# Optimization experiments

Measured on AMD Instinct MI355X. Metric: run time of the kernel, lower is better.

## Reference

```python
import jax, jax.numpy as jnp
import numpy as np

DIM = 256
HEADS = 8
WS = 8      # window size
SS = 4      # shift size
EPS = 1e-5
HEAD_DIM = DIM // HEADS
SCALE = HEAD_DIM ** (-0.5)
N = WS * WS

# relative position index, replicating tf.meshgrid default 'xy' indexing
_ch = np.arange(WS)
_coords = np.stack(np.meshgrid(_ch, _ch, indexing='xy'))          # [2, WS, WS]
_flat = _coords.reshape(2, -1)                                     # [2, N]
_rel = _flat[:, :, None] - _flat[:, None, :]                       # [2, N, N]
_rel = _rel.transpose(1, 2, 0) + np.array([WS - 1, WS - 1])
_rel = _rel * np.array([2 * WS - 1, 1])
RPI = jnp.asarray(_rel.sum(-1).reshape(-1))                        # [N*N] int


def _calc_mask(H, W):
    # faithful to source: mask is -100 where window region ids are EQUAL, 0 otherwise
    img = np.zeros((H, W))
    slices = (slice(0, -WS), slice(-WS, -SS), slice(-SS, None))
    cnt = 0
    for hs in slices:
        for ws_ in slices:
            img[hs, ws_] = cnt
            cnt += 1
    mw = img.reshape(H // WS, WS, W // WS, WS).transpose(0, 2, 1, 3).reshape(-1, N)
    diff = mw[:, None, :] - mw[:, :, None]
    mask = np.where(diff == 0, -100.0, 0.0).astype(np.float32)     # [nW, N, N]
    return jnp.asarray(mask)


def _layernorm(x, g, b):
    m = jnp.mean(x, axis=-1, keepdims=True)
    v = jnp.mean(jnp.square(x - m), axis=-1, keepdims=True)
    return (x - m) * jax.lax.rsqrt(v + EPS) * g + b


def setup_inputs() -> dict:
    key = jax.random.key(0)
    ks = jax.random.split(key, 8)
    B, L, C = 16, 64 * 64, DIM
    s = 0.02
    return {
        'x': jax.random.normal(ks[0], (B, L, C), jnp.float32),
        'norm1_g': jnp.ones((C,), jnp.float32),
        'norm1_b': jnp.zeros((C,), jnp.float32),
        'qkv_w': jax.random.normal(ks[1], (C, 3 * C), jnp.float32) * s,
        'qkv_b': jnp.zeros((3 * C,), jnp.float32),
        'rpb_table': jax.random.normal(ks[2], ((2 * WS - 1) ** 2, HEADS), jnp.float32) * s,
        'proj_w': jax.random.normal(ks[3], (C, C), jnp.float32) * s,
        'proj_b': jnp.zeros((C,), jnp.float32),
        'norm2_g': jnp.ones((C,), jnp.float32),
        'norm2_b': jnp.zeros((C,), jnp.float32),
        'fc1_w': jax.random.normal(ks[4], (C, 4 * C), jnp.float32) * s,
        'fc1_b': jnp.zeros((4 * C,), jnp.float32),
        'fc2_w': jax.random.normal(ks[5], (4 * C, C), jnp.float32) * s,
        'fc2_b': jnp.zeros((C,), jnp.float32),
        'h': 64,
        'w': 64,
    }


def reference(x, norm1_g, norm1_b, qkv_w, qkv_b, rpb_table, proj_w, proj_b,
              norm2_g, norm2_b, fc1_w, fc1_b, fc2_w, fc2_b, h, w):
    B, L, C = x.shape
    nH, nW = h // WS, w // WS
    nWin = nH * nW
    shortcut = x

    xn = _layernorm(x, norm1_g, norm1_b).reshape(B, h, w, C)
    xn = jnp.roll(xn, shift=(-SS, -SS), axis=(1, 2))                 # cyclic shift
    # window partition -> [B*nWin, N, C]
    xw = xn.reshape(B, nH, WS, nW, WS, C).transpose(0, 1, 3, 2, 4, 5).reshape(B * nWin, N, C)

    qkv = (xw @ qkv_w + qkv_b).reshape(B * nWin, N, 3, HEADS, HEAD_DIM)
    qkv = qkv.transpose(2, 0, 3, 1, 4)                               # [3, B*nWin, H, N, d]
    q, k, v = qkv[0] * SCALE, qkv[1], qkv[2]

    attn = jnp.einsum('bhnd,bhmd->bhnm', q, k)                       # [B*nWin, H, N, N]
    bias = rpb_table[RPI].reshape(N, N, HEADS).transpose(2, 0, 1)    # [H, N, N]
    attn = attn + bias[None]

    mask = _calc_mask(h, w)                                          # [nWin, N, N]
    attn = attn.reshape(B, nWin, HEADS, N, N) + mask[None, :, None]
    attn = jax.nn.softmax(attn, axis=-1).reshape(B * nWin, HEADS, N, N)

    out = jnp.einsum('bhnm,bhmd->bhnd', attn, v)                     # [B*nWin, H, N, d]
    out = out.transpose(0, 2, 1, 3).reshape(B * nWin, N, C)
    out = out @ proj_w + proj_b

    # window reverse + reverse shift
    out = out.reshape(B, nH, nW, WS, WS, C).transpose(0, 1, 3, 2, 4, 5).reshape(B, h, w, C)
    out = jnp.roll(out, shift=(SS, SS), axis=(1, 2)).reshape(B, h * w, C)

    y = shortcut + out
    m = _layernorm(y, norm2_g, norm2_b)
    m = jax.nn.gelu(m @ fc1_w + fc1_b, approximate=False) @ fc2_w + fc2_b
    # faithful to source: final residual reuses the ORIGINAL shortcut, not y
    return shortcut + m
```

## Files before the change

kernel.cpp:

```cpp
#include <hip/hip_runtime.h>
#include <math.h>

typedef __bf16 bf16;
typedef __bf16 bf16x4 __attribute__((ext_vector_type(4)));
typedef __bf16 bf16x8 __attribute__((ext_vector_type(8)));
typedef float f32x4 __attribute__((ext_vector_type(4)));

#define AS1 __attribute__((address_space(1)))
#define AS3 __attribute__((address_space(3)))

__device__ __forceinline__ void gload_lds16(const bf16* g, bf16* l) {
    __builtin_amdgcn_global_load_lds((const AS1 void*)g, (AS3 void*)l, 16, 0, 0);
}
__device__ __forceinline__ void gload_lds16c(const char* g, char* l) {
    __builtin_amdgcn_global_load_lds((const AS1 void*)g, (AS3 void*)l, 16, 0, 0);
}

__device__ __forceinline__ float gelu_fast(float v) {
    const float u = 1.5957691216057308f * (v + 0.044715f * v * v * v);
    return v / (1.0f + __expf(-u));
}

__device__ __forceinline__ unsigned cvt_fp8x4(float a, float b, float c, float d) {
    int r = 0;
    r = __builtin_amdgcn_cvt_pk_fp8_f32(a, b, r, false);
    r = __builtin_amdgcn_cvt_pk_fp8_f32(c, d, r, true);
    return (unsigned)r;
}

__global__ __launch_bounds__(256)
void wprep_all(const float* __restrict__ qkv_w, const float* __restrict__ proj_w,
               const float* __restrict__ fc1_w, const float* __restrict__ fc2_w,
               bf16* __restrict__ qkv_wt, bf16* __restrict__ proj_wt,
               bf16* __restrict__ fc1_wt, char* __restrict__ fc2_wq)
{
    int idx = blockIdx.x * 256 + threadIdx.x;
    if (idx < 524288) {
        const float* src; bf16* dst; int K, N;
        if (idx < 196608)      { src = qkv_w;  dst = qkv_wt;  K = 256; N = 768; }
        else if (idx < 262144) { idx -= 196608; src = proj_w; dst = proj_wt; K = 256; N = 256; }
        else                   { idx -= 262144; src = fc1_w;  dst = fc1_wt;  K = 256; N = 1024; }
        const int k = idx / N, n = idx % N;
        dst[(long)n * K + k] = (bf16)src[idx];
    } else {
        idx -= 524288;
        const int k = idx >> 8, n = idx & 255;
        const int r = __builtin_amdgcn_cvt_pk_fp8_f32(fc2_w[idx] * 16.0f, 0.f, 0, false);
        fc2_wq[(long)n * 1024 + k] = (char)(r & 0xFF);
    }
}

__global__ __launch_bounds__(256)
void ln1_window(const float* __restrict__ x, const float* __restrict__ g,
                const float* __restrict__ be, bf16* __restrict__ xw)
{
    const int t = threadIdx.x;
    const int lane = t & 63;
    const int w = t >> 6;
    const long tok = (long)blockIdx.x * 4 + w;
    const float4 v = ((const float4*)(x + tok * 256))[lane];
    float sum = v.x + v.y + v.z + v.w;
    float sq  = v.x * v.x + v.y * v.y + v.z * v.z + v.w * v.w;
#pragma unroll
    for (int m = 32; m >= 1; m >>= 1) {
        sum += __shfl_xor(sum, m, 64);
        sq  += __shfl_xor(sq,  m, 64);
    }
    const float mean = sum * (1.0f / 256.0f);
    const float var  = sq * (1.0f / 256.0f) - mean * mean;
    const float rstd = rsqrtf(var + 1e-5f);
    const float4 gv = ((const float4*)g)[lane];
    const float4 bv = ((const float4*)be)[lane];
    bf16x4 ov;
    ov[0] = (bf16)((v.x - mean) * rstd * gv.x + bv.x);
    ov[1] = (bf16)((v.y - mean) * rstd * gv.y + bv.y);
    ov[2] = (bf16)((v.z - mean) * rstd * gv.z + bv.z);
    ov[3] = (bf16)((v.w - mean) * rstd * gv.w + bv.w);
    const int b = (int)(tok >> 12);
    const int l = (int)(tok & 4095);
    const int i = l >> 6, j = l & 63;
    const int ip = (i + 60) & 63, jp = (j + 60) & 63;
    const int winl = ((ip >> 3) << 3) + (jp >> 3);
    const int n = ((ip & 7) << 3) + (jp & 7);
    const long drow = ((long)b * 64 + winl) * 64 + n;
    *(bf16x4*)(xw + drow * 256 + lane * 4) = ov;
}

template<int EPI, int KT>
__global__ __launch_bounds__(512, 2)
void gemm_w(const bf16* __restrict__ A, const bf16* __restrict__ Bt,
            const float* __restrict__ bias, void* __restrict__ outp,
            int N, const float* __restrict__ xres, void* __restrict__ aux,
            int gx, int nb)
{
    constexpr int K = KT * 32;
    extern __shared__ bf16 lds[];
    bf16* sA = lds;
    bf16* sB = lds + 3 * 8192;
    const int t = threadIdx.x;
    const int l = t & 63;
    const int w = t >> 6;
    const int wr = w >> 1, wc = w & 1;
    const int q = nb >> 3;
    const int id = ((int)blockIdx.x & 7) * q + ((int)blockIdx.x >> 3);
    const long m0 = (long)(id / gx) * 256;
    const long n0 = (long)(id % gx) * 128;

    const bf16* asrcp[2]; bf16* adstp[2];
#pragma unroll
    for (int j = 0; j < 2; j++) {
        const int idx = j * 512 + t;
        const int p = idx >> 3, s = idx & 7;
        const int sl = s ^ (p & 7);
        const int row = 2 * p + (sl >> 2);
        const int ce = (sl & 3) * 8;
        asrcp[j] = A + (m0 + row) * (long)K + ce;
        adstp[j] = &sA[idx * 8];
    }
    const bf16* bsrcp; bf16* bdstp;
    {
        const int p = t >> 3, s = t & 7;
        const int sl = s ^ (p & 7);
        const int row = 2 * p + (sl >> 2);
        const int ce = (sl & 3) * 8;
        bsrcp = Bt + (n0 + row) * (long)K + ce;
        bdstp = &sB[t * 8];
    }

    const int c = l >> 4;
    int eA[4], eB[4];
#pragma unroll
    for (int i = 0; i < 4; i++) {
        const int rowA = wr * 64 + (l & 15) + i * 16;
        const int pa = rowA >> 1;
        eA[i] = (pa * 8 + ((((rowA & 1) << 2) + c) ^ (pa & 7))) * 8;
        const int rowB = wc * 64 + (l & 15) + i * 16;
        const int pb = rowB >> 1;
        eB[i] = (pb * 8 + ((((rowB & 1) << 2) + c) ^ (pb & 7))) * 8;
    }

    f32x4 acc[4][4];
#pragma unroll
    for (int i = 0; i < 4; i++)
#pragma unroll
        for (int j = 0; j < 4; j++) acc[i][j] = (f32x4){0.f, 0.f, 0.f, 0.f};

#define STAGE(bufi, ko)                                                        \
    do {                                                                       \
        gload_lds16(asrcp[0] + (ko), adstp[0] + (bufi) * 8192);                \
        gload_lds16(asrcp[1] + (ko), adstp[1] + (bufi) * 8192);                \
        gload_lds16(bsrcp + (ko), bdstp + (bufi) * 4096);                      \
    } while (0)

    STAGE(0, 0);
    STAGE(1, 32);

#pragma unroll
    for (int kt = 0; kt < KT; ++kt) {
        const int buf = kt % 3;
        if (kt < KT - 1)
            asm volatile("s_waitcnt vmcnt(3)" ::: "memory");
        else
            asm volatile("s_waitcnt vmcnt(0)" ::: "memory");
        __builtin_amdgcn_s_barrier();
        __builtin_amdgcn_sched_barrier(0);
        if (kt + 2 < KT)
            STAGE((kt + 2) % 3, (kt + 2) * 32);
        bf16x8 av[4], bv[4];
#pragma unroll
        for (int ni = 0; ni < 4; ni++)
            bv[ni] = *(const bf16x8*)&sB[buf * 4096 + eB[ni]];
#pragma unroll
        for (int mi = 0; mi < 4; mi++)
            av[mi] = *(const bf16x8*)&sA[buf * 8192 + eA[mi]];
#pragma unroll
        for (int mi = 0; mi < 4; mi++)
#pragma unroll
            for (int ni = 0; ni < 4; ni++)
                acc[mi][ni] = __builtin_amdgcn_mfma_f32_16x16x32_bf16(
                    bv[ni], av[mi], acc[mi][ni], 0, 0, 0);
    }
#undef STAGE

    if constexpr (EPI == 2) {
        __syncthreads();
        char* wlds = (char*)(lds) + w * 4608;
#pragma unroll
        for (int mi = 0; mi < 4; mi++)
#pragma unroll
            for (int ni = 0; ni < 4; ni++) {
                const int colb = ni * 16 + (l >> 4) * 4;
                const int rowl = mi * 16 + (l & 15);
                const float4 bz = *(const float4*)&bias[n0 + wc * 64 + colb];
                const unsigned pk = cvt_fp8x4(
                    gelu_fast(acc[mi][ni][0] + bz.x) * 16.0f,
                    gelu_fast(acc[mi][ni][1] + bz.y) * 16.0f,
                    gelu_fast(acc[mi][ni][2] + bz.z) * 16.0f,
                    gelu_fast(acc[mi][ni][3] + bz.w) * 16.0f);
                *(unsigned*)(wlds + rowl * 72 + colb) = pk;
            }
        char* outb = (char*)outp;
#pragma unroll
        for (int j = 0; j < 8; j++) {
            const int r = j * 8 + (l >> 3);
            const long vr = *(const long*)(wlds + r * 72 + (l & 7) * 8);
            const long row = m0 + wr * 64 + r;
            *(long*)&outb[row * (long)N + n0 + wc * 64 + (l & 7) * 8] = vr;
        }
    } else {
        const bool transpose_path = (n0 < 512);
        if (transpose_path) {
            __syncthreads();
            char* wlds = (char*)(lds) + w * 8704;
#pragma unroll
            for (int mi = 0; mi < 4; mi++)
#pragma unroll
                for (int ni = 0; ni < 4; ni++) {
                    const int colb = (ni * 16 + (l >> 4) * 4) * 2;
                    const int rowl = mi * 16 + (l & 15);
                    const float4 bz = *(const float4*)&bias[n0 + wc * 64 + ni * 16 + (l >> 4) * 4];
                    bf16x4 ov;
                    ov[0] = (bf16)(acc[mi][ni][0] + bz.x);
                    ov[1] = (bf16)(acc[mi][ni][1] + bz.y);
                    ov[2] = (bf16)(acc[mi][ni][2] + bz.z);
                    ov[3] = (bf16)(acc[mi][ni][3] + bz.w);
                    *(bf16x4*)(wlds + rowl * 136 + (colb ^ ((rowl & 7) << 4))) = ov;
                }
            bf16* outb = (bf16*)outp;
#pragma unroll
            for (int j = 0; j < 8; j++) {
                const int r = j * 8 + (l >> 3);
                const bf16x8 vr = *(const bf16x8*)(wlds + r * 136 + (((l & 7) * 16) ^ ((r & 7) << 4)));
                const long row = m0 + wr * 64 + r;
                const int col = (int)(n0 + wc * 64 + (l & 7) * 8);
                *(bf16x8*)&outb[row * N + col] = vr;
            }
        } else {
#pragma unroll
            for (int mi = 0; mi < 4; mi++)
#pragma unroll
                for (int ni = 0; ni < 4; ni++) {
                    const long row = m0 + wr * 64 + mi * 16 + (l & 15);
                    const int col = (int)(n0 + wc * 64 + ni * 16 + (l >> 4) * 4);
                    const float4 bz = *(const float4*)&bias[col];
                    bf16* vt = (bf16*)aux;
                    const int win = (int)(row >> 6);
                    const int n = (int)(row & 63);
#pragma unroll
                    for (int j = 0; j < 4; j++)
                        vt[(long)win * 16384 + (col - 512 + j) * 64 + n] =
                            (bf16)(acc[mi][ni][j] + ((const float*)&bz)[j]);
                }
        }
    }
    (void)xres; (void)aux;
}

__global__ __launch_bounds__(512, 2)
void gemm_fc2(const char* __restrict__ A, const char* __restrict__ Bq,
              const float* __restrict__ bias, float* __restrict__ out,
              const float* __restrict__ xres, int nb)
{
    constexpr int KT = 32;
    extern __shared__ char lds8[];
    char* sA8 = lds8;
    char* sB8 = lds8 + 3 * 8192;
    const int t = threadIdx.x;
    const int l = t & 63;
    const int w = t >> 6;
    const int wr = w >> 1, wc = w & 1;
    const int q = nb >> 3;
    const int id = ((int)blockIdx.x & 7) * q + ((int)blockIdx.x >> 3);
    const long m0 = (long)(id / 2) * 256;
    const long n0 = (long)(id % 2) * 128;

    const char* asrc; char* adst;
    {
        const int g = t >> 4, s = t & 15;
        const int r = s >> 1;
        const int h = (s & 1) ^ ((r >> 2) & 1);
        const int row = g * 8 + r;
        asrc = A + (m0 + row) * 1024 + h * 16;
        adst = sA8 + t * 16;
    }
    const char* bsrc = nullptr; char* bdst = nullptr;
    if (t < 256) {
        const int g = t >> 4, s = t & 15;
        const int r = s >> 1;
        const int h = (s & 1) ^ ((r >> 2) & 1);
        const int row = g * 8 + r;
        bsrc = Bq + (n0 + row) * 1024 + h * 16;
        bdst = sB8 + t * 16;
    }

    const int c = l >> 4;
    int eA[4], eB[4];
#pragma unroll
    for (int i = 0; i < 4; i++) {
        const int rowA = wr * 64 + (l & 15) + i * 16;
        const int rA = rowA & 7;
        eA[i] = (rowA >> 3) * 256 + (2 * rA + ((c >> 1) ^ ((rA >> 2) & 1))) * 16 + (c & 1) * 8;
        const int rowB = wc * 64 + (l & 15) + i * 16;
        const int rB = rowB & 7;
        eB[i] = (rowB >> 3) * 256 + (2 * rB + ((c >> 1) ^ ((rB >> 2) & 1))) * 16 + (c & 1) * 8;
    }

    f32x4 acc[4][4];
#pragma unroll
    for (int i = 0; i < 4; i++)
#pragma unroll
        for (int j = 0; j < 4; j++) acc[i][j] = (f32x4){0.f, 0.f, 0.f, 0.f};

#define STAGE2(bufi, ko)                                                       \
    do {                                                                       \
        gload_lds16c(asrc + (ko), adst + (bufi) * 8192);                       \
        if (t < 256) gload_lds16c(bsrc + (ko), bdst + (bufi) * 4096);          \
    } while (0)

    STAGE2(0, 0);
    STAGE2(1, 32);

#pragma unroll
    for (int kt = 0; kt < KT; ++kt) {
        const int buf = kt % 3;
        if (kt < KT - 1) {
            if (w < 4) asm volatile("s_waitcnt vmcnt(2)" ::: "memory");
            else       asm volatile("s_waitcnt vmcnt(1)" ::: "memory");
        } else {
            asm volatile("s_waitcnt vmcnt(0)" ::: "memory");
        }
        __builtin_amdgcn_s_barrier();
        __builtin_amdgcn_sched_barrier(0);
        if (kt + 2 < KT)
            STAGE2((kt + 2) % 3, (kt + 2) * 32);
        long av[4], bv[4];
#pragma unroll
        for (int ni = 0; ni < 4; ni++)
            bv[ni] = *(const long*)&sB8[buf * 4096 + eB[ni]];
#pragma unroll
        for (int mi = 0; mi < 4; mi++)
            av[mi] = *(const long*)&sA8[buf * 8192 + eA[mi]];
#pragma unroll
        for (int mi = 0; mi < 4; mi++)
#pragma unroll
            for (int ni = 0; ni < 4; ni++)
                acc[mi][ni] = __builtin_amdgcn_mfma_f32_16x16x32_fp8_fp8(
                    bv[ni], av[mi], acc[mi][ni], 0, 0, 0);
    }
#undef STAGE2

#pragma unroll
    for (int mi = 0; mi < 4; mi++)
#pragma unroll
        for (int ni = 0; ni < 4; ni++) {
            const long row = m0 + wr * 64 + mi * 16 + (l & 15);
            const int col = (int)(n0 + wc * 64 + ni * 16 + (l >> 4) * 4);
            const float4 bz = *(const float4*)&bias[col];
            const float4 xr = *(const float4*)&xres[row * 256 + col];
            float4 ov;
            ov.x = acc[mi][ni][0] * 0.00390625f + bz.x + xr.x;
            ov.y = acc[mi][ni][1] * 0.00390625f + bz.y + xr.y;
            ov.z = acc[mi][ni][2] * 0.00390625f + bz.z + xr.z;
            ov.w = acc[mi][ni][3] * 0.00390625f + bz.w + xr.w;
            *(float4*)&out[row * 256 + col] = ov;
        }
}

__global__ __launch_bounds__(512, 2)
void proj_ln2(const bf16* __restrict__ A, const bf16* __restrict__ Bt,
              const float* __restrict__ bias, const float* __restrict__ x,
              const float* __restrict__ g2, const float* __restrict__ b2,
              bf16* __restrict__ xn2, int nb)
{
    extern __shared__ bf16 lds[];
    bf16* sA = lds;
    bf16* sB = lds + 3 * 4096;
    float* sred = (float*)(lds + 3 * 4096 + 3 * 8192);
    const int t = threadIdx.x;
    const int l = t & 63;
    const int w = t >> 6;
    const int wr = w >> 2, wc = w & 3;
    const int q = nb >> 3;
    const int id = ((int)blockIdx.x & 7) * q + ((int)blockIdx.x >> 3);
    const long m0 = (long)id * 128;

    const bf16* asrcp; bf16* adstp;
    {
        const int p = t >> 3, s = t & 7;
        const int sl = s ^ (p & 7);
        const int row = 2 * p + (sl >> 2);
        const int ce = (sl & 3) * 8;
        asrcp = A + (m0 + row) * 256 + ce;
        adstp = &sA[t * 8];
    }
    const bf16* bsrcp[2]; bf16* bdstp[2];
#pragma unroll
    for (int j = 0; j < 2; j++) {
        const int idx = j * 512 + t;
        const int p = idx >> 3, s = idx & 7;
        const int sl = s ^ (p & 7);
        const int row = 2 * p + (sl >> 2);
        const int ce = (sl & 3) * 8;
        bsrcp[j] = Bt + (long)row * 256 + ce;
        bdstp[j] = &sB[idx * 8];
    }

    const int c = l >> 4;
    int eA[4], eB[4];
#pragma unroll
    for (int i = 0; i < 4; i++) {
        const int rowA = wr * 64 + (l & 15) + i * 16;
        const int pa = rowA >> 1;
        eA[i] = (pa * 8 + ((((rowA & 1) << 2) + c) ^ (pa & 7))) * 8;
        const int rowB = wc * 64 + (l & 15) + i * 16;
        const int pb = rowB >> 1;
        eB[i] = (pb * 8 + ((((rowB & 1) << 2) + c) ^ (pb & 7))) * 8;
    }

    f32x4 acc[4][4];
#pragma unroll
    for (int i = 0; i < 4; i++)
#pragma unroll
        for (int j = 0; j < 4; j++) acc[i][j] = (f32x4){0.f, 0.f, 0.f, 0.f};

#define STAGE(bufi, ko)                                                        \
    do {                                                                       \
        gload_lds16(asrcp + (ko), adstp + (bufi) * 4096);                      \
        gload_lds16(bsrcp[0] + (ko), bdstp[0] + (bufi) * 8192);                \
        gload_lds16(bsrcp[1] + (ko), bdstp[1] + (bufi) * 8192);                \
    } while (0)

    STAGE(0, 0);
    STAGE(1, 32);

#pragma unroll
    for (int kt = 0; kt < 8; ++kt) {
        const int buf = kt % 3;
        if (kt < 7)
            asm volatile("s_waitcnt vmcnt(3)" ::: "memory");
        else
            asm volatile("s_waitcnt vmcnt(0)" ::: "memory");
        __builtin_amdgcn_s_barrier();
        __builtin_amdgcn_sched_barrier(0);
        if (kt + 2 < 8)
            STAGE((kt + 2) % 3, (kt + 2) * 32);
        bf16x8 av[4], bv[4];
#pragma unroll
        for (int ni = 0; ni < 4; ni++)
            bv[ni] = *(const bf16x8*)&sB[buf * 8192 + eB[ni]];
#pragma unroll
        for (int mi = 0; mi < 4; mi++)
            av[mi] = *(const bf16x8*)&sA[buf * 4096 + eA[mi]];
#pragma unroll
        for (int mi = 0; mi < 4; mi++)
#pragma unroll
            for (int ni = 0; ni < 4; ni++)
                acc[mi][ni] = __builtin_amdgcn_mfma_f32_16x16x32_bf16(
                    bv[ni], av[mi], acc[mi][ni], 0, 0, 0);
    }
#undef STAGE

    float ts[4] = {0.f, 0.f, 0.f, 0.f}, tq[4] = {0.f, 0.f, 0.f, 0.f};
    long tok[4];
#pragma unroll
    for (int mi = 0; mi < 4; mi++) {
        const long row = m0 + wr * 64 + mi * 16 + (l & 15);
        const int gwin = (int)(row >> 6);
        const int n = (int)(row & 63);
        const int bb = gwin >> 6, wi = gwin & 63;
        const int ipp = ((wi >> 3) << 3) + (n >> 3);
        const int jpp = ((wi & 7) << 3) + (n & 7);
        const int ii = (ipp + 4) & 63, jj = (jpp + 4) & 63;
        tok[mi] = ((long)bb << 12) + (ii << 6) + jj;
#pragma unroll
        for (int ni = 0; ni < 4; ni++) {
            const int col = wc * 64 + ni * 16 + (l >> 4) * 4;
            const float4 bz = *(const float4*)&bias[col];
            const float4 xr = *(const float4*)&x[tok[mi] * 256 + col];
            acc[mi][ni][0] += bz.x + xr.x;
            acc[mi][ni][1] += bz.y + xr.y;
            acc[mi][ni][2] += bz.z + xr.z;
            acc[mi][ni][3] += bz.w + xr.w;
#pragma unroll
            for (int j = 0; j < 4; j++) {
                ts[mi] += acc[mi][ni][j];
                tq[mi] += acc[mi][ni][j] * acc[mi][ni][j];
            }
        }
    }
#pragma unroll
    for (int mi = 0; mi < 4; mi++) {
        ts[mi] += __shfl_xor(ts[mi], 16, 64);
        tq[mi] += __shfl_xor(tq[mi], 16, 64);
        ts[mi] += __shfl_xor(ts[mi], 32, 64);
        tq[mi] += __shfl_xor(tq[mi], 32, 64);
    }
    if (l < 16) {
#pragma unroll
        for (int mi = 0; mi < 4; mi++) {
            const int r = wr * 64 + mi * 16 + l;
            sred[r * 9 + wc * 2]     = ts[mi];
            sred[r * 9 + wc * 2 + 1] = tq[mi];
        }
    }
    __syncthreads();
#pragma unroll
    for (int mi = 0; mi < 4; mi++) {
        const int r = wr * 64 + mi * 16 + (l & 15);
        float S = 0.f, Q = 0.f;
#pragma unroll
        for (int k = 0; k < 4; k++) {
            S += sred[r * 9 + k * 2];
            Q += sred[r * 9 + k * 2 + 1];
        }
        const float mean = S * (1.0f / 256.0f);
        const float var  = Q * (1.0f / 256.0f) - mean * mean;
        const float rstd = rsqrtf(var + 1e-5f);
#pragma unroll
        for (int ni = 0; ni < 4; ni++) {
            const int col = wc * 64 + ni * 16 + (l >> 4) * 4;
            const float4 gg = *(const float4*)&g2[col];
            const float4 bb = *(const float4*)&b2[col];
            bf16x4 ov;
            ov[0] = (bf16)((acc[mi][ni][0] - mean) * rstd * gg.x + bb.x);
            ov[1] = (bf16)((acc[mi][ni][1] - mean) * rstd * gg.y + bb.y);
            ov[2] = (bf16)((acc[mi][ni][2] - mean) * rstd * gg.z + bb.z);
            ov[3] = (bf16)((acc[mi][ni][3] - mean) * rstd * gg.w + bb.w);
            *(bf16x4*)&xn2[tok[mi] * 256 + col] = ov;
        }
    }
}

__global__ __launch_bounds__(256, 4)
void attn_kernel(const bf16* __restrict__ qkv, const bf16* __restrict__ vT,
                 const float* __restrict__ rpb, bf16* __restrict__ out)
{
    __shared__ bf16 P_lds[4][64 * 64];
    const int t = threadIdx.x;
    const int lane = t & 63;
    const int w = t >> 6;
    const int win = blockIdx.x >> 1;
    const int head = (blockIdx.x & 1) * 4 + w;
    const int wi = win & 63;
    const int lr = lane & 15;
    const int lg = lane >> 4;
    const int lk = lg * 8;
    const long base = (long)win * 64 * 768;
    const float scale = 0.17677669529663687f;
    const int whb = (wi >> 3) << 3;
    const int wwb = (wi & 7) << 3;
    const f32x4 z4 = {0.f, 0.f, 0.f, 0.f};

    const bf16* qp  = qkv + base + head * 32;
    const bf16* kp  = qkv + base + 256 + head * 32;
    const bf16* vtp = vT + (long)win * 16384 + head * 32 * 64;

    int idm[4];
#pragma unroll
    for (int ni = 0; ni < 4; ni++) {
        const int m = ni * 16 + lr;
        const int gi2 = whb + (m >> 3), gj2 = wwb + (m & 7);
        idm[ni] = (gi2 < 56 ? 0 : (gi2 < 60 ? 1 : 2)) * 3 + (gj2 < 56 ? 0 : (gj2 < 60 ? 1 : 2));
    }

    bf16x8 aq[4], bk[4];
#pragma unroll
    for (int mi = 0; mi < 4; mi++)
        aq[mi] = *(const bf16x8*)(qp + (mi * 16 + lr) * 768 + lk);
#pragma unroll
    for (int ni = 0; ni < 4; ni++)
        bk[ni] = *(const bf16x8*)(kp + (ni * 16 + lr) * 768 + lk);

    f32x4 s[4][4];
#pragma unroll
    for (int i = 0; i < 4; i++)
#pragma unroll
        for (int j = 0; j < 4; j++) s[i][j] = z4;
#pragma unroll
    for (int mi = 0; mi < 4; mi++)
#pragma unroll
        for (int ni = 0; ni < 4; ni++)
            s[mi][ni] = __builtin_amdgcn_mfma_f32_16x16x32_bf16(aq[mi], bk[ni], s[mi][ni], 0, 0, 0);

#pragma unroll
    for (int mi = 0; mi < 4; mi++)
#pragma unroll
        for (int r = 0; r < 4; r++) {
            const int n = mi * 16 + lg * 4 + r;
            const int gi = whb + (n >> 3);
            const int gj = wwb + (n & 7);
            const int idn = (gi < 56 ? 0 : (gi < 60 ? 1 : 2)) * 3 + (gj < 56 ? 0 : (gj < 60 ? 1 : 2));
            float vals[4];
            float rowmax = -3.0e38f;
#pragma unroll
            for (int ni = 0; ni < 4; ni++) {
                const int m = ni * 16 + lr;
                const int dj = (n & 7) - (m & 7);
                const int di = (n >> 3) - (m >> 3);
                float sv = s[mi][ni][r] * scale + rpb[((dj + 7) * 15 + (di + 7)) * 8 + head];
                if (idn == idm[ni]) sv -= 100.0f;
                vals[ni] = sv;
                rowmax = fmaxf(rowmax, sv);
            }
#pragma unroll
            for (int msk = 8; msk >= 1; msk >>= 1)
                rowmax = fmaxf(rowmax, __shfl_xor(rowmax, msk, 64));
            float rsum = 0.f;
#pragma unroll
            for (int ni = 0; ni < 4; ni++) {
                const float p = __expf(vals[ni] - rowmax);
                vals[ni] = p;
                rsum += p;
            }
#pragma unroll
            for (int msk = 8; msk >= 1; msk >>= 1)
                rsum += __shfl_xor(rsum, msk, 64);
            const float inv = 1.0f / rsum;
            const int swz = (n & 7) << 3;
#pragma unroll
            for (int ni = 0; ni < 4; ni++)
                P_lds[w][n * 64 + ((ni * 16 + lr) ^ swz)] = (bf16)(vals[ni] * inv);
        }

    f32x4 o[4][2];
#pragma unroll
    for (int i = 0; i < 4; i++)
#pragma unroll
        for (int j = 0; j < 2; j++) o[i][j] = z4;
#pragma unroll
    for (int kk = 0; kk < 2; kk++) {
        bf16x8 bv[2];
#pragma unroll
        for (int ni = 0; ni < 2; ni++)
            bv[ni] = *(const bf16x8*)&vtp[(ni * 16 + lr) * 64 + kk * 32 + lk];
#pragma unroll
        for (int mi = 0; mi < 4; mi++) {
            const int row = mi * 16 + lr;
            const bf16x8 ap = *(const bf16x8*)&P_lds[w][row * 64 + ((kk * 32 + lk) ^ ((row & 7) << 3))];
#pragma unroll
            for (int ni = 0; ni < 2; ni++)
                o[mi][ni] = __builtin_amdgcn_mfma_f32_16x16x32_bf16(bv[ni], ap, o[mi][ni], 0, 0, 0);
        }
    }
#pragma unroll
    for (int mi = 0; mi < 4; mi++)
#pragma unroll
        for (int ni = 0; ni < 2; ni++) {
            const int n = mi * 16 + lr;
            const int d = ni * 16 + lg * 4;
            bf16x4 ov;
            ov[0] = (bf16)o[mi][ni][0]; ov[1] = (bf16)o[mi][ni][1];
            ov[2] = (bf16)o[mi][ni][2]; ov[3] = (bf16)o[mi][ni][3];
            *(bf16x4*)(out + ((long)(win * 64 + n)) * 256 + head * 32 + d) = ov;
        }
}

extern "C" void kernel_launch(void* const* d_in, const int* in_sizes, int n_in,
                              void* d_out, int out_size, void* d_ws, size_t ws_size,
                              hipStream_t stream)
{
    (void)in_sizes; (void)n_in; (void)out_size;
    const float* x      = (const float*)d_in[0];
    const float* n1g    = (const float*)d_in[1];
    const float* n1b    = (const float*)d_in[2];
    const float* qkv_w  = (const float*)d_in[3];
    const float* qkv_b  = (const float*)d_in[4];
    const float* rpb    = (const float*)d_in[5];
    const float* proj_w = (const float*)d_in[6];
    const float* proj_b = (const float*)d_in[7];
    const float* n2g    = (const float*)d_in[8];
    const float* n2b    = (const float*)d_in[9];
    const float* fc1_w  = (const float*)d_in[10];
    const float* fc1_b  = (const float*)d_in[11];
    const float* fc2_w  = (const float*)d_in[12];
    const float* fc2_b  = (const float*)d_in[13];
    float* out = (float*)d_out;

    char* ws = (char*)d_ws;
    bf16* qkv_wt  = (bf16*)(ws + 0);
    bf16* proj_wt = (bf16*)(ws + 393216);
    bf16* fc1_wt  = (bf16*)(ws + 524288);
    char* fc2_wq  = (char*)(ws + 1048576);
    bf16* xw      = (bf16*)(ws + 2097152);
    bf16* qkvb    = (bf16*)(ws + 35651584);
    bf16* attn_o  = xw;
    bf16* vT      = (bf16*)d_out;
    bf16* xn2     = (bf16*)d_out + 16777216;
    char* hbuf8   = (char*)(ws + 2097152);
    if (ws_size < 136314880ull) return;

    const size_t LB  = 73728;
    const size_t LBP = 78336;
    const size_t LBF = 36864;

    wprep_all<<<3072, 256, 0, stream>>>(qkv_w, proj_w, fc1_w, fc2_w,
                                        qkv_wt, proj_wt, fc1_wt, fc2_wq);

    ln1_window<<<16384, 256, 0, stream>>>(x, n1g, n1b, xw);
    gemm_w<0, 8><<<1536, 512, LB, stream>>>(xw, qkv_wt, qkv_b, qkvb, 768, nullptr, vT, 6, 1536);
    attn_kernel<<<2048, 256, 0, stream>>>(qkvb, vT, rpb, attn_o);
    proj_ln2<<<512, 512, LBP, stream>>>(attn_o, proj_wt, proj_b, x, n2g, n2b, xn2, 512);
    gemm_w<2, 8><<<2048, 512, LB, stream>>>(xn2, fc1_wt, fc1_b, hbuf8, 1024, nullptr, nullptr, 8, 2048);
    gemm_fc2<<<512, 512, LBF, stream>>>(hbuf8, fc2_wq, fc2_b, out, x, 512);
}
```

Before: 274.8 us.

## Store fc1 output in MFMA fragment-tiled layout and stage V transposes through LDS

The fc1 epilogue now writes fp8 GELU outputs directly in a per-wave 64x64 fragment-tiled layout, which removes the LDS round trip and the barrier. The fc2 kernel's A loader and LDS fragment reads change to match this tiled layout, reading two 4-byte pieces per operand. The V-transpose epilogue of the qkv GEMM now goes through LDS so it can do vectorized 16-byte global stores instead of scattered 2-byte writes. The risks are a more complex producer/consumer layout contract between the kernels and extra LDS reads in the fc2 inner loop.

```diff
diff --git a/kernel.cpp b/kernel.cpp
--- a/kernel.cpp
+++ b/kernel.cpp
@@ -183,30 +183,20 @@
 #undef STAGE
 
     if constexpr (EPI == 2) {
-        __syncthreads();
-        char* wlds = (char*)(lds) + w * 4608;
+        char* outb = (char*)outp;
+        const long tbase = (((m0 >> 6) + wr) * (N >> 6) + (n0 >> 6) + wc) * 4096;
 #pragma unroll
         for (int mi = 0; mi < 4; mi++)
 #pragma unroll
             for (int ni = 0; ni < 4; ni++) {
-                const int colb = ni * 16 + (l >> 4) * 4;
-                const int rowl = mi * 16 + (l & 15);
-                const float4 bz = *(const float4*)&bias[n0 + wc * 64 + colb];
+                const float4 bz = *(const float4*)&bias[n0 + wc * 64 + ni * 16 + (l >> 4) * 4];
                 const unsigned pk = cvt_fp8x4(
                     gelu_fast(acc[mi][ni][0] + bz.x) * 16.0f,
                     gelu_fast(acc[mi][ni][1] + bz.y) * 16.0f,
                     gelu_fast(acc[mi][ni][2] + bz.z) * 16.0f,
                     gelu_fast(acc[mi][ni][3] + bz.w) * 16.0f);
-                *(unsigned*)(wlds + rowl * 72 + colb) = pk;
+                *(unsigned*)&outb[tbase + (mi * 4 + ni) * 256 + l * 4] = pk;
             }
-        char* outb = (char*)outp;
-#pragma unroll
-        for (int j = 0; j < 8; j++) {
-            const int r = j * 8 + (l >> 3);
-            const long vr = *(const long*)(wlds + r * 72 + (l & 7) * 8);
-            const long row = m0 + wr * 64 + r;
-            *(long*)&outb[row * (long)N + n0 + wc * 64 + (l & 7) * 8] = vr;
-        }
     } else {
         const bool transpose_path = (n0 < 512);
         if (transpose_path) {
@@ -236,21 +226,29 @@
                 *(bf16x8*)&outb[row * N + col] = vr;
             }
         } else {
+            __syncthreads();
+            char* wlds = (char*)(lds) + w * 8704;
 #pragma unroll
             for (int mi = 0; mi < 4; mi++)
 #pragma unroll
                 for (int ni = 0; ni < 4; ni++) {
-                    const long row = m0 + wr * 64 + mi * 16 + (l & 15);
-                    const int col = (int)(n0 + wc * 64 + ni * 16 + (l >> 4) * 4);
-                    const float4 bz = *(const float4*)&bias[col];
-                    bf16* vt = (bf16*)aux;
-                    const int win = (int)(row >> 6);
-                    const int n = (int)(row & 63);
+                    const int drel0 = ni * 16 + (l >> 4) * 4;
+                    const int n = mi * 16 + (l & 15);
+                    const float4 bz = *(const float4*)&bias[n0 + wc * 64 + drel0];
 #pragma unroll
                     for (int j = 0; j < 4; j++)
-                        vt[(long)win * 16384 + (col - 512 + j) * 64 + n] =
+                        *(bf16*)(wlds + (drel0 + j) * 136 + n * 2) =
                             (bf16)(acc[mi][ni][j] + ((const float*)&bz)[j]);
                 }
+            bf16* vt = (bf16*)aux;
+            const int win = (int)(m0 >> 6) + wr;
+            const int dbase = (int)(n0 - 512) + wc * 64;
+#pragma unroll
+            for (int j2 = 0; j2 < 8; j2++) {
+                const int drel = j2 * 8 + (l >> 3);
+                const bf16x8 vv = *(const bf16x8*)(wlds + drel * 136 + (l & 7) * 16);
+                *(bf16x8*)(vt + (long)win * 16384 + (dbase + drel) * 64 + (l & 7) * 8) = vv;
+            }
         }
     }
     (void)xres; (void)aux;
@@ -276,11 +274,10 @@
 
     const char* asrc; char* adst;
     {
-        const int g = t >> 4, s = t & 15;
-        const int r = s >> 1;
-        const int h = (s & 1) ^ ((r >> 2) & 1);
-        const int row = g * 8 + r;
-        asrc = A + (m0 + row) * 1024 + h * 16;
+        const int tile = t >> 7, r = t & 127;
+        const int sub = r >> 4, chIn = r & 15;
+        const int fragb = (sub >> 1) * 4 + (sub & 1);
+        asrc = A + ((m0 >> 6) + tile) * 16 * 4096 + fragb * 256 + chIn * 16;
         adst = sA8 + t * 16;
     }
     const char* bsrc = nullptr; char* bdst = nullptr;
@@ -293,13 +290,17 @@
         bdst = sB8 + t * 16;
     }
 
+    const int g2 = l >> 4;
+    const int nrel = g2 >> 1;
+    const int ga = (g2 & 1) * 2;
+    int eA2[4];
+#pragma unroll
+    for (int i = 0; i < 4; i++)
+        eA2[i] = wr * 2048 + (i * 2 + nrel) * 256 + (ga * 16 + (l & 15)) * 4;
     const int c = l >> 4;
-    int eA[4], eB[4];
+    int eB[4];
 #pragma unroll
     for (int i = 0; i < 4; i++) {
-        const int rowA = wr * 64 + (l & 15) + i * 16;
-        const int rA = rowA & 7;
-        eA[i] = (rowA >> 3) * 256 + (2 * rA + ((c >> 1) ^ ((rA >> 2) & 1))) * 16 + (c & 1) * 8;
         const int rowB = wc * 64 + (l & 15) + i * 16;
         const int rB = rowB & 7;
         eB[i] = (rowB >> 3) * 256 + (2 * rB + ((c >> 1) ^ ((rB >> 2) & 1))) * 16 + (c & 1) * 8;
@@ -311,14 +312,15 @@
 #pragma unroll
         for (int j = 0; j < 4; j++) acc[i][j] = (f32x4){0.f, 0.f, 0.f, 0.f};
 
-#define STAGE2(bufi, ko)                                                       \
+#define STAGE2(bufi, kt_)                                                      \
     do {                                                                       \
-        gload_lds16c(asrc + (ko), adst + (bufi) * 8192);                       \
-        if (t < 256) gload_lds16c(bsrc + (ko), bdst + (bufi) * 4096);          \
+        gload_lds16c(asrc + ((kt_) >> 1) * 4096 + ((kt_) & 1) * 512,           \
+                     adst + (bufi) * 8192);                                    \
+        if (t < 256) gload_lds16c(bsrc + (kt_) * 32, bdst + (bufi) * 4096);    \
     } while (0)
 
     STAGE2(0, 0);
-    STAGE2(1, 32);
+    STAGE2(1, 1);
 
 #pragma unroll
     for (int kt = 0; kt < KT; ++kt) {
@@ -332,14 +334,17 @@
         __builtin_amdgcn_s_barrier();
         __builtin_amdgcn_sched_barrier(0);
         if (kt + 2 < KT)
-            STAGE2((kt + 2) % 3, (kt + 2) * 32);
+            STAGE2((kt + 2) % 3, kt + 2);
         long av[4], bv[4];
 #pragma unroll
         for (int ni = 0; ni < 4; ni++)
             bv[ni] = *(const long*)&sB8[buf * 4096 + eB[ni]];
 #pragma unroll
-        for (int mi = 0; mi < 4; mi++)
-            av[mi] = *(const long*)&sA8[buf * 8192 + eA[mi]];
+        for (int mi = 0; mi < 4; mi++) {
+            const unsigned u0 = *(const unsigned*)&sA8[buf * 8192 + eA2[mi]];
+            const unsigned u1 = *(const unsigned*)&sA8[buf * 8192 + eA2[mi] + 64];
+            av[mi] = (long)(((unsigned long long)u1 << 32) | u0);
+        }
 #pragma unroll
         for (int mi = 0; mi < 4; mi++)
 #pragma unroll
```

Result: no change. 276.7 us (+0.7%).
